# Optimization experiments

Measured on AMD Instinct MI355X. Metric: run time of the kernel, lower is better.

The kernel has to match this reference:

```python
import jax, jax.numpy as jnp
import numpy as np


def setup_inputs() -> dict:
    key = jax.random.key(0)
    ks = jax.random.split(key, 3)
    B, D, H, K = 16384, 256, 8192, 32
    x = jax.random.normal(ks[0], (B, D), dtype=jnp.float32)
    W_enc = jax.random.normal(ks[1], (H, D), dtype=jnp.float32) * (1.0 / np.sqrt(D))
    b_enc = jnp.zeros((H,), dtype=jnp.float32)
    # W_dec initialized as encoder weight clone, then row-normalized to unit norm
    W_dec = jax.random.normal(ks[2], (H, D), dtype=jnp.float32)
    W_dec = W_dec / (jnp.linalg.norm(W_dec, axis=1, keepdims=True) + jnp.finfo(jnp.float32).eps)
    b_dec = jnp.zeros((D,), dtype=jnp.float32)
    return {"x": x, "W_enc": W_enc, "b_enc": b_enc, "W_dec": W_dec, "b_dec": b_dec, "k": K}


def reference(x, W_enc, b_enc, W_dec, b_dec, k):
    B, D = x.shape
    H = W_enc.shape[0]
    # encoder: sae_in = x - b_dec; pre_acts = relu(Linear(sae_in))
    sae_in = x - b_dec
    pre_acts = jax.nn.relu(sae_in @ W_enc.T + b_enc)  # [B, H]
    # top-k activation over hidden dim
    topk_vals, topk_idx = jax.lax.top_k(pre_acts, k)  # [B, k]
    # per-latent activation counts (bincount over flattened indices)
    counts = jnp.zeros((H,), dtype=jnp.float32).at[topk_idx.reshape(-1)].add(1.0)
    # scatter top-k values into sparse latent tensor
    rows = jnp.arange(B)[:, None]
    z = jnp.zeros_like(pre_acts).at[rows, topk_idx].set(topk_vals)  # [B, H]
    # decode
    x_reconstructed = z @ W_dec + b_dec  # [B, D]
    # fvu stat
    e = x_reconstructed - x
    total_variance = jnp.sum((x - x.mean(0)) ** 2)
    fvu = jnp.sum(e ** 2) / total_variance
    return x_reconstructed, counts, fvu
```

## Files before the change

### kernel.cpp

```cpp
#include <hip/hip_runtime.h>

typedef unsigned short u16;
typedef unsigned int   u32;
typedef unsigned long long u64;

typedef __bf16 bf16x8 __attribute__((ext_vector_type(8)));
typedef float  f32x4  __attribute__((ext_vector_type(4)));

#define B_ROWS   16384
#define D_DIM    256
#define H_DIM    8192
#define THR_C    2.35f
#define QCAP     48

#define SAE_OFF    0u
#define WENCB_OFF  8388608u
#define WDECB_OFF  12582912u
#define TROW_OFF   16777216u
#define CAND_OFF   16842752u
#define CGQ_OFF    29425664u
#define COLSUM_OFF 29687808u
#define SUMSQ_OFF  29688832u
#define SSE_OFF    29688836u

__device__ __forceinline__ u16 f2bf(float f) {
  u32 u = __float_as_uint(f);
  u32 r = (u + 0x7fffu + ((u >> 16) & 1u)) >> 16;
  return (u16)r;
}
__device__ __forceinline__ float bf2f(u16 h) {
  return __uint_as_float(((u32)h) << 16);
}

__device__ __forceinline__ void async_copy16(const void* g, void* l) {
  __builtin_amdgcn_global_load_lds((const __attribute__((address_space(1))) u32*)g,
                                   (__attribute__((address_space(3))) u32*)l,
                                   16, 0, 0);
}

__global__ void k_zero(float* counts_out, float* accums) {
  int i = blockIdx.x * 256 + threadIdx.x;
  if (i < H_DIM + 1) counts_out[i] = 0.f;
  if (i < 258) accums[i] = 0.f;
}

__global__ __launch_bounds__(256) void k_prep_x(const float* __restrict__ x,
                                                const float* __restrict__ bdec,
                                                u16* __restrict__ sae,
                                                float* __restrict__ trow,
                                                float* __restrict__ colsum,
                                                float* __restrict__ sumsq) {
  __shared__ float cssh[256];
  __shared__ float sqsh[4];
  const int tid = threadIdx.x;
  const int l = tid & 63, w = tid >> 6;
  const float4 bd4 = *(const float4*)(bdec + l * 4);
  float4 cs4 = {0.f, 0.f, 0.f, 0.f};
  float sq = 0.f;
  for (int i = 0; i < 8; ++i) {
    const int row = blockIdx.x * 32 + w * 8 + i;
    const float4 x4 = *(const float4*)(x + (size_t)row * D_DIM + l * 4);
    float4 s4 = {x4.x - bd4.x, x4.y - bd4.y, x4.z - bd4.z, x4.w - bd4.w};
    ushort4 o;
    o.x = f2bf(s4.x); o.y = f2bf(s4.y); o.z = f2bf(s4.z); o.w = f2bf(s4.w);
    *(ushort4*)(sae + (size_t)row * D_DIM + l * 4) = o;
    cs4.x += x4.x; cs4.y += x4.y; cs4.z += x4.z; cs4.w += x4.w;
    sq += x4.x * x4.x + x4.y * x4.y + x4.z * x4.z + x4.w * x4.w;
    float ss = s4.x * s4.x + s4.y * s4.y + s4.z * s4.z + s4.w * s4.w;
#pragma unroll
    for (int off = 32; off > 0; off >>= 1) ss += __shfl_xor(ss, off);
    if (l == 0) trow[row] = THR_C * sqrtf(ss * (1.0f / 256.0f));
  }
  if (w == 0) { cssh[l * 4 + 0] = cs4.x; cssh[l * 4 + 1] = cs4.y; cssh[l * 4 + 2] = cs4.z; cssh[l * 4 + 3] = cs4.w; }
  __syncthreads();
#pragma unroll
  for (int ww = 1; ww < 4; ++ww) {
    if (w == ww) { cssh[l * 4 + 0] += cs4.x; cssh[l * 4 + 1] += cs4.y; cssh[l * 4 + 2] += cs4.z; cssh[l * 4 + 3] += cs4.w; }
    __syncthreads();
  }
#pragma unroll
  for (int off = 32; off > 0; off >>= 1) sq += __shfl_xor(sq, off);
  if (l == 0) sqsh[w] = sq;
  __syncthreads();
  atomicAdd(&colsum[tid], cssh[tid]);
  if (tid == 0) atomicAdd(sumsq, sqsh[0] + sqsh[1] + sqsh[2] + sqsh[3]);
}

__global__ __launch_bounds__(256) void k_prep_w(const float4* __restrict__ wenc,
                                                const float4* __restrict__ wdec,
                                                ushort4* __restrict__ wencb,
                                                ushort4* __restrict__ wdecb) {
  int i = blockIdx.x * 256 + threadIdx.x;
  const int half = H_DIM * D_DIM / 4;
  float4 v;
  if (i < half) v = wenc[i]; else v = wdec[i - half];
  ushort4 o;
  o.x = f2bf(v.x); o.y = f2bf(v.y); o.z = f2bf(v.z); o.w = f2bf(v.w);
  if (i < half) wencb[i] = o; else wdecb[i - half] = o;
}

__global__ __launch_bounds__(512, 4) void k_gemm(const u16* __restrict__ sae,
                                                 const u16* __restrict__ wenc,
                                                 const float* __restrict__ benc,
                                                 const float* __restrict__ trow,
                                                 u32* __restrict__ cand,
                                                 u32* __restrict__ cgq) {
  __shared__ __align__(16) u16 ldsw[2][8192];
  __shared__ u32 lcand[128 * QCAP];
  __shared__ u32 lcnt[128];
  const int tid = threadIdx.x;
  const int l   = tid & 63;
  const int w   = tid >> 6;
  const int bid = blockIdx.x;
  const int q   = bid & 3;
  const int m   = bid >> 2;
  const int wr  = w & 3;
  const int wc  = w >> 2;
  const int rbase = m * 128 + wr * 32;
  const int kc  = l >> 4;
  const int r16 = l & 15;

  if (tid < 128) lcnt[tid] = 0u;

  bf16x8 a[2][8];
#pragma unroll
  for (int fr = 0; fr < 2; ++fr) {
    const u16* ap = sae + (size_t)(rbase + fr * 16 + r16) * 256 + kc * 8;
#pragma unroll
    for (int ks = 0; ks < 8; ++ks)
      a[fr][ks] = *(const bf16x8*)(ap + ks * 32);
  }
  float trw[2][4];
#pragma unroll
  for (int fr = 0; fr < 2; ++fr)
#pragma unroll
    for (int rr = 0; rr < 4; ++rr)
      trw[fr][rr] = trow[rbase + fr * 16 + kc * 4 + rr];

  const char* wbytes = (const char*)wenc;
  auto stage = [&](int ci, int buf) {
    const int gcol0 = q * 2048 + ci * 32;
#pragma unroll
    for (int i = 0; i < 2; ++i) {
      int L    = i * 8192 + tid * 16;
      int col  = L >> 9;
      int pblk = (L >> 4) & 31;
      int cblk = pblk ^ (col & 15);
      const void* src = wbytes + (size_t)(gcol0 + col) * 512 + (size_t)cblk * 16;
      void* dst = (char*)(&ldsw[buf][0]) + i * 8192 + w * 1024;
      async_copy16(src, dst);
    }
  };

  stage(0, 0);
  __syncthreads();

  const f32x4 fzero = {0.f, 0.f, 0.f, 0.f};
  for (int ci = 0; ci < 64; ++ci) {
    const int cur = ci & 1;
    if (ci + 1 < 64) stage(ci + 1, cur ^ 1);
    const int gcol0 = q * 2048 + ci * 32;
    const char* bufc = (const char*)(&ldsw[cur][0]);

    const float be = benc[gcol0 + wc * 16 + r16];

    f32x4 acc[2];
    acc[0] = fzero; acc[1] = fzero;

#pragma unroll
    for (int ks = 0; ks < 8; ++ks) {
      const int colL = wc * 16 + r16;
      const int pb = (ks * 4 + kc) ^ r16;
      const bf16x8 bfrag = *(const bf16x8*)(bufc + (size_t)colL * 512 + (size_t)pb * 16);
#pragma unroll
      for (int fr = 0; fr < 2; ++fr)
        acc[fr] = __builtin_amdgcn_mfma_f32_16x16x32_bf16(a[fr][ks], bfrag, acc[fr], 0, 0, 0);
    }

#pragma unroll
    for (int fr = 0; fr < 2; ++fr) {
#pragma unroll
      for (int rr = 0; rr < 4; ++rr) {
        float v = acc[fr][rr] + be;
        if (v > trw[fr][rr]) {
          const int rowl = wr * 32 + fr * 16 + kc * 4 + rr;
          const int colg = gcol0 + wc * 16 + r16;
          u32 pos = atomicAdd(&lcnt[rowl], 1u);
          if (pos < (u32)QCAP)
            lcand[rowl * QCAP + pos] = ((u32)f2bf(v) << 16) | (u32)colg;
        }
      }
    }
    __syncthreads();
  }

  if (tid < 128) cgq[(size_t)(m * 128 + tid) * 4 + q] = lcnt[tid];
  const int rowl = tid >> 2;
  const u32 cnt = lcnt[rowl];
  const u32 lim = cnt < (u32)QCAP ? cnt : (u32)QCAP;
  u32* dst = cand + ((size_t)(m * 128 + rowl) * 4 + q) * QCAP;
#pragma unroll
  for (int j = 0; j < QCAP / 4; ++j) {
    const u32 s = (u32)(tid & 3) + 4u * j;
    if (s < lim) dst[s] = lcand[rowl * QCAP + s];
  }
}

__device__ __forceinline__ u64 sort64(u64 v, int l) {
#pragma unroll
  for (int k = 2; k <= 64; k <<= 1) {
#pragma unroll
    for (int j = k >> 1; j > 0; j >>= 1) {
      u64 o = __shfl_xor(v, j);
      const bool up    = ((l & k) == 0);
      const bool lower = ((l & j) == 0);
      u64 mn = v < o ? v : o;
      u64 mx = v < o ? o : v;
      v = (up == lower) ? mn : mx;
    }
  }
  return v;
}
__device__ __forceinline__ u32 sort64u(u32 v, int l) {
#pragma unroll
  for (int k = 2; k <= 64; k <<= 1) {
#pragma unroll
    for (int j = k >> 1; j > 0; j >>= 1) {
      u32 o = __shfl_xor(v, j);
      const bool up    = ((l & k) == 0);
      const bool lower = ((l & j) == 0);
      u32 mn = v < o ? v : o;
      u32 mx = v < o ? o : v;
      v = (up == lower) ? mn : mx;
    }
  }
  return v;
}

__global__ __launch_bounds__(256) void k_seldec(const u32* __restrict__ cand,
                                                const u32* __restrict__ cgq,
                                                const u16* __restrict__ sae,
                                                const u16* __restrict__ wenc,
                                                const float* __restrict__ benc,
                                                const float* __restrict__ wencf,
                                                const u16* __restrict__ wdecb,
                                                const float* __restrict__ bdec,
                                                const float* __restrict__ x,
                                                float* __restrict__ out,
                                                float* __restrict__ counts,
                                                float* __restrict__ sse) {
  __shared__ float sh_s[4][256];
  __shared__ float essh[4];
  const int l = threadIdx.x & 63;
  const int w = threadIdx.x >> 6;
  const int row = blockIdx.x * 4 + w;
  const float4 x4  = *(const float4*)(x + (size_t)row * D_DIM + l * 4);
  const float4 bd4 = *(const float4*)(bdec + l * 4);
  {
    float4 s4 = {x4.x - bd4.x, x4.y - bd4.y, x4.z - bd4.z, x4.w - bd4.w};
    *(float4*)(&sh_s[w][l * 4]) = s4;
  }

  const uint4 c4 = *(const uint4*)(cgq + (size_t)row * 4);
  const bool ovf = (c4.x > (u32)QCAP) | (c4.y > (u32)QCAP) | (c4.z > (u32)QCAP) | (c4.w > (u32)QCAP);
  const u32 cum0 = c4.x, cum1 = cum0 + c4.y, cum2 = cum1 + c4.z;
  const u32 T = cum2 + c4.w;
  u64 v;
  if (!ovf && T >= 32u) {
    const u32* cb = cand + (size_t)row * 4 * QCAP;
    auto fetch = [&](u32 p) -> u32 {
      u32 qi, off;
      if (p < cum0)      { qi = 0; off = p; }
      else if (p < cum1) { qi = 1; off = p - cum0; }
      else if (p < cum2) { qi = 2; off = p - cum1; }
      else               { qi = 3; off = p - cum2; }
      return cb[qi * QCAP + off];
    };
    u32 key = ((u32)l < T) ? fetch((u32)l) : 0u;
    key = sort64u(key, l);
    for (u32 p = 64; p < T; p += 64) {
      const u32 pp = p + (u32)l;
      u32 u = (pp < T) ? fetch(pp) : 0u;
      u = sort64u(u, l);
      u32 ur = __shfl(u, 63 - l);
      key = key > ur ? key : ur;
      key = sort64u(key, l);
    }
    v = key ? ((((u64)(key & 0xffff0000u)) << 32) | (u64)(key & 0x1fffu)) : 0ull;
    const int g  = l >> 4;
    const int gl = l & 15;
    const float* srow = &sh_s[w][gl * 16];
    const float4 sv0 = *(const float4*)(srow + 0);
    const float4 sv1 = *(const float4*)(srow + 4);
    const float4 sv2 = *(const float4*)(srow + 8);
    const float4 sv3 = *(const float4*)(srow + 12);
    auto cscore = [&](int j) -> float {
      const u32 kj = (u32)__shfl((int)key, 24 + g * 4 + j);
      const u32 ti = kj & 0x1fffu;
      const float* wrow = wencf + (size_t)ti * D_DIM + gl * 16;
      const float4 w0 = *(const float4*)(wrow + 0);
      const float4 w1 = *(const float4*)(wrow + 4);
      const float4 w2 = *(const float4*)(wrow + 8);
      const float4 w3 = *(const float4*)(wrow + 12);
      float p = sv0.x * w0.x + sv0.y * w0.y + sv0.z * w0.z + sv0.w * w0.w
              + sv1.x * w1.x + sv1.y * w1.y + sv1.z * w1.z + sv1.w * w1.w
              + sv2.x * w2.x + sv2.y * w2.y + sv2.z * w2.z + sv2.w * w2.w
              + sv3.x * w3.x + sv3.y * w3.y + sv3.z * w3.z + sv3.w * w3.w;
      p += __shfl_xor(p, 1);
      p += __shfl_xor(p, 2);
      p += __shfl_xor(p, 4);
      p += __shfl_xor(p, 8);
      return p;
    };
    const float r0 = cscore(0);
    const float r1 = cscore(1);
    const float r2 = cscore(2);
    const float r3 = cscore(3);
    {
      const int c  = (l - 24) & 63;
      const int sg = ((c >> 2) & 3) * 16;
      const float t0 = __shfl(r0, sg);
      const float t1 = __shfl(r1, sg);
      const float t2 = __shfl(r2, sg);
      const float t3 = __shfl(r3, sg);
      const int cm = c & 3;
      const float ps = cm == 0 ? t0 : (cm == 1 ? t1 : (cm == 2 ? t2 : t3));
      if (l >= 24 && l < 40 && key != 0u) {
        const u32 ti = key & 0x1fffu;
        const float ns = fmaxf(ps + benc[ti], 0.f);
        v = ((u64)__float_as_uint(ns) << 32) | ti;
      }
    }
    v = sort64(v, l);
  } else {
    v = 0ull;
    const u16* ap = sae + (size_t)row * 256;
    for (int c0 = 0; c0 < H_DIM; c0 += 64) {
      const int col = c0 + l;
      const u16* wp = wenc + (size_t)col * 256;
      float s = benc[col];
      for (int kk = 0; kk < 256; ++kk) s += bf2f(ap[kk]) * bf2f(wp[kk]);
      s = fmaxf(s, 0.f);
      u64 u = ((u64)__float_as_uint(s) << 32) | (u32)col;
      u = sort64(u, l);
      if (c0 == 0) {
        v = u;
      } else {
        u64 ur = __shfl(u, 63 - l);
        v = v > ur ? v : ur;
        v = sort64(v, l);
      }
    }
  }
  if (l >= 32) {
    const u32 idx = (u32)(v & 0xffffffffu);
    atomicAdd(&counts[idx], 1.0f);
  }
  float ax = 0.f, ay = 0.f, az = 0.f, aw2 = 0.f;
#pragma unroll 8
  for (int j = 0; j < 32; ++j) {
    const u64 t = __shfl(v, 32 + j);
    const float tv = __uint_as_float((u32)(t >> 32));
    const u32 ti = (u32)(t & 0x1fffu);
    const ushort4 wv = *(const ushort4*)(wdecb + (size_t)ti * 256 + l * 4);
    ax += tv * bf2f(wv.x); ay += tv * bf2f(wv.y);
    az += tv * bf2f(wv.z); aw2 += tv * bf2f(wv.w);
  }
  float4 xr;
  xr.x = ax + bd4.x; xr.y = ay + bd4.y; xr.z = az + bd4.z; xr.w = aw2 + bd4.w;
  *(float4*)(out + (size_t)row * 256 + l * 4) = xr;
  const float e0 = xr.x - x4.x, e1 = xr.y - x4.y, e2 = xr.z - x4.z, e3 = xr.w - x4.w;
  float es = e0 * e0 + e1 * e1 + e2 * e2 + e3 * e3;
#pragma unroll
  for (int off = 32; off > 0; off >>= 1) es += __shfl_xor(es, off);
  if (l == 0) essh[w] = es;
  __syncthreads();
  if (threadIdx.x == 0) atomicAdd(sse, essh[0] + essh[1] + essh[2] + essh[3]);
}

__global__ __launch_bounds__(256) void k_fvu(const float* __restrict__ colsum,
                                             const float* __restrict__ sumsq,
                                             const float* __restrict__ sse,
                                             float* __restrict__ out) {
  __shared__ float red[4];
  const int tid = threadIdx.x;
  const int l = tid & 63;
  const int w = tid >> 6;
  const float c = colsum[tid];
  float p = c * c;
#pragma unroll
  for (int off = 32; off > 0; off >>= 1) p += __shfl_xor(p, off);
  if (l == 0) red[w] = p;
  __syncthreads();
  if (tid == 0) {
    const float tv = sumsq[0] - (red[0] + red[1] + red[2] + red[3]) * (1.0f / 16384.0f);
    out[(size_t)B_ROWS * D_DIM + H_DIM] = sse[0] / tv;
  }
}

extern "C" void kernel_launch(void* const* d_in, const int* in_sizes, int n_in,
                              void* d_out, int out_size, void* d_ws, size_t ws_size,
                              hipStream_t stream) {
  (void)in_sizes; (void)n_in; (void)out_size; (void)ws_size;
  const float* x     = (const float*)d_in[0];
  const float* W_enc = (const float*)d_in[1];
  const float* b_enc = (const float*)d_in[2];
  const float* W_dec = (const float*)d_in[3];
  const float* b_dec = (const float*)d_in[4];
  float* out = (float*)d_out;
  char* ws = (char*)d_ws;

  u16*  sae    = (u16*)(ws + SAE_OFF);
  u16*  wencb  = (u16*)(ws + WENCB_OFF);
  u16*  wdecb  = (u16*)(ws + WDECB_OFF);
  float* trowp = (float*)(ws + TROW_OFF);
  u32*  candp  = (u32*)(ws + CAND_OFF);
  u32*  cgqp   = (u32*)(ws + CGQ_OFF);
  float* colsum = (float*)(ws + COLSUM_OFF);
  float* sumsq  = (float*)(ws + SUMSQ_OFF);
  float* ssep   = (float*)(ws + SSE_OFF);
  float* counts = out + (size_t)B_ROWS * D_DIM;

  hipLaunchKernelGGL(k_zero,   dim3(33),   dim3(256), 0, stream, counts, colsum);
  hipLaunchKernelGGL(k_prep_x, dim3(512),  dim3(256), 0, stream, x, b_dec, sae, trowp, colsum, sumsq);
  hipLaunchKernelGGL(k_prep_w, dim3(4096), dim3(256), 0, stream,
                     (const float4*)W_enc, (const float4*)W_dec, (ushort4*)wencb, (ushort4*)wdecb);
  hipLaunchKernelGGL(k_gemm,   dim3(512),  dim3(512), 0, stream, sae, wencb, b_enc, trowp, candp, cgqp);
  hipLaunchKernelGGL(k_seldec, dim3(4096), dim3(256), 0, stream, candp, cgqp, sae, wencb, b_enc, W_enc, wdecb, b_dec, x, out, counts, ssep);
  hipLaunchKernelGGL(k_fvu,    dim3(1),    dim3(256), 0, stream, colsum, sumsq, ssep, out);
}
```

Baseline: 217.0 us.

## Switch encoder GEMM to 32x32x16 MFMA with 256-row tiles per block

The encoder GEMM now uses 32x32x16 bf16 MFMA instructions, with two independent accumulators that are summed in the epilogue. The block row tile grows from 128 to 256 rows: each wave owns 32 rows across all 32 columns of a chunk, and the grid is halved. Each staged W_enc tile is reused across twice as many rows, cutting LDS and global weight traffic per output, and the larger MFMA shape gives better throughput per instruction. In exchange it holds more registers (16 A fragments and two 16-wide accumulators), uses more LDS for the candidate lists, and lowers the occupancy hint to 2, with only 256 blocks to fill the GPU.

```diff
diff --git a/kernel.cpp b/kernel.cpp
--- a/kernel.cpp
+++ b/kernel.cpp
@@ -6,6 +6,7 @@
 
 typedef __bf16 bf16x8 __attribute__((ext_vector_type(8)));
 typedef float  f32x4  __attribute__((ext_vector_type(4)));
+typedef float  f32x16 __attribute__((ext_vector_type(16)));
 
 #define B_ROWS   16384
 #define D_DIM    256
@@ -99,43 +100,37 @@
   if (i < half) wencb[i] = o; else wdecb[i - half] = o;
 }
 
-__global__ __launch_bounds__(512, 4) void k_gemm(const u16* __restrict__ sae,
+__global__ __launch_bounds__(512, 2) void k_gemm(const u16* __restrict__ sae,
                                                  const u16* __restrict__ wenc,
                                                  const float* __restrict__ benc,
                                                  const float* __restrict__ trow,
                                                  u32* __restrict__ cand,
                                                  u32* __restrict__ cgq) {
   __shared__ __align__(16) u16 ldsw[2][8192];
-  __shared__ u32 lcand[128 * QCAP];
-  __shared__ u32 lcnt[128];
+  __shared__ u32 lcand[256 * QCAP];
+  __shared__ u32 lcnt[256];
   const int tid = threadIdx.x;
   const int l   = tid & 63;
   const int w   = tid >> 6;
-  const int bid = blockIdx.x;
-  const int q   = bid & 3;
-  const int m   = bid >> 2;
-  const int wr  = w & 3;
-  const int wc  = w >> 2;
-  const int rbase = m * 128 + wr * 32;
-  const int kc  = l >> 4;
-  const int r16 = l & 15;
-
-  if (tid < 128) lcnt[tid] = 0u;
-
-  bf16x8 a[2][8];
-#pragma unroll
-  for (int fr = 0; fr < 2; ++fr) {
-    const u16* ap = sae + (size_t)(rbase + fr * 16 + r16) * 256 + kc * 8;
-#pragma unroll
-    for (int ks = 0; ks < 8; ++ks)
-      a[fr][ks] = *(const bf16x8*)(ap + ks * 32);
-  }
-  float trw[2][4];
-#pragma unroll
-  for (int fr = 0; fr < 2; ++fr)
-#pragma unroll
-    for (int rr = 0; rr < 4; ++rr)
-      trw[fr][rr] = trow[rbase + fr * 16 + kc * 4 + rr];
+  const int q   = blockIdx.x & 3;
+  const int m   = blockIdx.x >> 2;
+  const int rbase = m * 256 + w * 32;
+  const int r32 = l & 31;
+  const int h   = l >> 5;
+
+  if (tid < 256) lcnt[tid] = 0u;
+
+  bf16x8 a[16];
+  {
+    const u16* ap = sae + (size_t)(rbase + r32) * 256 + h * 8;
+#pragma unroll
+    for (int ks = 0; ks < 16; ++ks)
+      a[ks] = *(const bf16x8*)(ap + ks * 16);
+  }
+  float trw[16];
+#pragma unroll
+  for (int r = 0; r < 16; ++r)
+    trw[r] = trow[rbase + (r & 3) + 8 * (r >> 2) + 4 * h];
 
   const char* wbytes = (const char*)wenc;
   auto stage = [&](int ci, int buf) {
@@ -155,53 +150,47 @@
   stage(0, 0);
   __syncthreads();
 
-  const f32x4 fzero = {0.f, 0.f, 0.f, 0.f};
   for (int ci = 0; ci < 64; ++ci) {
     const int cur = ci & 1;
     if (ci + 1 < 64) stage(ci + 1, cur ^ 1);
     const int gcol0 = q * 2048 + ci * 32;
     const char* bufc = (const char*)(&ldsw[cur][0]);
 
-    const float be = benc[gcol0 + wc * 16 + r16];
-
-    f32x4 acc[2];
-    acc[0] = fzero; acc[1] = fzero;
-
-#pragma unroll
-    for (int ks = 0; ks < 8; ++ks) {
-      const int colL = wc * 16 + r16;
-      const int pb = (ks * 4 + kc) ^ r16;
-      const bf16x8 bfrag = *(const bf16x8*)(bufc + (size_t)colL * 512 + (size_t)pb * 16);
-#pragma unroll
-      for (int fr = 0; fr < 2; ++fr)
-        acc[fr] = __builtin_amdgcn_mfma_f32_16x16x32_bf16(a[fr][ks], bfrag, acc[fr], 0, 0, 0);
-    }
-
-#pragma unroll
-    for (int fr = 0; fr < 2; ++fr) {
-#pragma unroll
-      for (int rr = 0; rr < 4; ++rr) {
-        float v = acc[fr][rr] + be;
-        if (v > trw[fr][rr]) {
-          const int rowl = wr * 32 + fr * 16 + kc * 4 + rr;
-          const int colg = gcol0 + wc * 16 + r16;
-          u32 pos = atomicAdd(&lcnt[rowl], 1u);
-          if (pos < (u32)QCAP)
-            lcand[rowl * QCAP + pos] = ((u32)f2bf(v) << 16) | (u32)colg;
-        }
+    const float be = benc[gcol0 + r32];
+
+    f32x16 acc0 = {0.f}, acc1 = {0.f};
+#pragma unroll
+    for (int ks = 0; ks < 16; ks += 2) {
+      const int pb0 = ((ks + 0) * 2 + h) ^ (l & 15);
+      const int pb1 = ((ks + 1) * 2 + h) ^ (l & 15);
+      const bf16x8 b0 = *(const bf16x8*)(bufc + (size_t)r32 * 512 + (size_t)pb0 * 16);
+      const bf16x8 b1 = *(const bf16x8*)(bufc + (size_t)r32 * 512 + (size_t)pb1 * 16);
+      acc0 = __builtin_amdgcn_mfma_f32_32x32x16_bf16(a[ks + 0], b0, acc0, 0, 0, 0);
+      acc1 = __builtin_amdgcn_mfma_f32_32x32x16_bf16(a[ks + 1], b1, acc1, 0, 0, 0);
+    }
+
+#pragma unroll
+    for (int r = 0; r < 16; ++r) {
+      const float v = acc0[r] + acc1[r] + be;
+      if (v > trw[r]) {
+        const int rowl = w * 32 + (r & 3) + 8 * (r >> 2) + 4 * h;
+        const int colg = gcol0 + r32;
+        u32 pos = atomicAdd(&lcnt[rowl], 1u);
+        if (pos < (u32)QCAP)
+          lcand[rowl * QCAP + pos] = ((u32)f2bf(v) << 16) | (u32)colg;
       }
     }
     __syncthreads();
   }
 
-  if (tid < 128) cgq[(size_t)(m * 128 + tid) * 4 + q] = lcnt[tid];
-  const int rowl = tid >> 2;
+  if (tid < 256) cgq[(size_t)(m * 256 + tid) * 4 + q] = lcnt[tid];
+  const int rowl = tid >> 1;
   const u32 cnt = lcnt[rowl];
   const u32 lim = cnt < (u32)QCAP ? cnt : (u32)QCAP;
-  u32* dst = cand + ((size_t)(m * 128 + rowl) * 4 + q) * QCAP;
-#pragma unroll
-  for (int j = 0; j < QCAP / 4; ++j) {
-    const u32 s = (u32)(tid & 3) + 4u * j;
+  u32* dst = cand + ((size_t)(m * 256 + rowl) * 4 + q) * QCAP;
+#pragma unroll
+  for (int j = 0; j < QCAP / 2; ++j) {
+    const u32 s = (u32)(tid & 1) + 2u * j;
     if (s < lim) dst[s] = lcand[rowl * QCAP + s];
   }
 }
@@ -425,7 +414,7 @@
   hipLaunchKernelGGL(k_prep_x, dim3(512),  dim3(256), 0, stream, x, b_dec, sae, trowp, colsum, sumsq);
   hipLaunchKernelGGL(k_prep_w, dim3(4096), dim3(256), 0, stream,
                      (const float4*)W_enc, (const float4*)W_dec, (ushort4*)wencb, (ushort4*)wdecb);
-  hipLaunchKernelGGL(k_gemm,   dim3(512),  dim3(512), 0, stream, sae, wencb, b_enc, trowp, candp, cgqp);
+  hipLaunchKernelGGL(k_gemm,   dim3(256),  dim3(512), 0, stream, sae, wencb, b_enc, trowp, candp, cgqp);
   hipLaunchKernelGGL(k_seldec, dim3(4096), dim3(256), 0, stream, candp, cgqp, sae, wencb, b_enc, W_enc, wdecb, b_dec, x, out, counts, ssep);
   hipLaunchKernelGGL(k_fvu,    dim3(1),    dim3(256), 0, stream, colsum, sumsq, ssep, out);
 }
```

Result: slower. 249.3 us (+14.9%).

## Retile encoder GEMM to 256-row blocks over 8 column splits

Applied to the files above, without the earlier changes.

The encoder GEMM now gives each block 256 rows and one eighth of the hidden columns, using 4 waves of 64 rows each instead of 8 waves of 32 rows. Each block stages 16 weight columns per step, so every B fragment loaded from LDS feeds four MFMAs instead of two, and the LDS staging buffers shrink. The candidate buffer is split into 8 per-row segments with a smaller per-segment cap, and the select kernel is updated to read the 8 counts and index across the 8 segments. The smaller cap makes per-segment overflow more likely, which sends those rows to the slow exact fallback path. The higher register use of the larger A tile may also reduce occupancy.

```diff
diff --git a/kernel.cpp b/kernel.cpp
--- a/kernel.cpp
+++ b/kernel.cpp
@@ -11,17 +11,17 @@
 #define D_DIM    256
 #define H_DIM    8192
 #define THR_C    2.35f
-#define QCAP     48
+#define QCAP     28
 
 #define SAE_OFF    0u
 #define WENCB_OFF  8388608u
 #define WDECB_OFF  12582912u
 #define TROW_OFF   16777216u
 #define CAND_OFF   16842752u
-#define CGQ_OFF    29425664u
-#define COLSUM_OFF 29687808u
-#define SUMSQ_OFF  29688832u
-#define SSE_OFF    29688836u
+#define CGQ_OFF    31522816u
+#define COLSUM_OFF 32047104u
+#define SUMSQ_OFF  32048128u
+#define SSE_OFF    32048132u
 
 __device__ __forceinline__ u16 f2bf(float f) {
   u32 u = __float_as_uint(f);
@@ -99,55 +99,52 @@
   if (i < half) wencb[i] = o; else wdecb[i - half] = o;
 }
 
-__global__ __launch_bounds__(512, 4) void k_gemm(const u16* __restrict__ sae,
+__global__ __launch_bounds__(256, 2) void k_gemm(const u16* __restrict__ sae,
                                                  const u16* __restrict__ wenc,
                                                  const float* __restrict__ benc,
                                                  const float* __restrict__ trow,
                                                  u32* __restrict__ cand,
                                                  u32* __restrict__ cgq) {
-  __shared__ __align__(16) u16 ldsw[2][8192];
-  __shared__ u32 lcand[128 * QCAP];
-  __shared__ u32 lcnt[128];
+  __shared__ __align__(16) u16 ldsw[2][4096];
+  __shared__ u32 lcand[256 * QCAP];
+  __shared__ u32 lcnt[256];
   const int tid = threadIdx.x;
   const int l   = tid & 63;
   const int w   = tid >> 6;
-  const int bid = blockIdx.x;
-  const int q   = bid & 3;
-  const int m   = bid >> 2;
-  const int wr  = w & 3;
-  const int wc  = w >> 2;
-  const int rbase = m * 128 + wr * 32;
+  const int q   = blockIdx.x & 7;
+  const int m   = blockIdx.x >> 3;
+  const int rbase = m * 256 + w * 64;
   const int kc  = l >> 4;
   const int r16 = l & 15;
 
-  if (tid < 128) lcnt[tid] = 0u;
-
-  bf16x8 a[2][8];
-#pragma unroll
-  for (int fr = 0; fr < 2; ++fr) {
+  lcnt[tid] = 0u;
+
+  bf16x8 a[4][8];
+#pragma unroll
+  for (int fr = 0; fr < 4; ++fr) {
     const u16* ap = sae + (size_t)(rbase + fr * 16 + r16) * 256 + kc * 8;
 #pragma unroll
     for (int ks = 0; ks < 8; ++ks)
       a[fr][ks] = *(const bf16x8*)(ap + ks * 32);
   }
-  float trw[2][4];
-#pragma unroll
-  for (int fr = 0; fr < 2; ++fr)
+  float trw[4][4];
+#pragma unroll
+  for (int fr = 0; fr < 4; ++fr)
 #pragma unroll
     for (int rr = 0; rr < 4; ++rr)
       trw[fr][rr] = trow[rbase + fr * 16 + kc * 4 + rr];
 
   const char* wbytes = (const char*)wenc;
   auto stage = [&](int ci, int buf) {
-    const int gcol0 = q * 2048 + ci * 32;
+    const int gcol0 = q * 1024 + ci * 16;
 #pragma unroll
     for (int i = 0; i < 2; ++i) {
-      int L    = i * 8192 + tid * 16;
+      int L    = i * 4096 + tid * 16;
       int col  = L >> 9;
       int pblk = (L >> 4) & 31;
-      int cblk = pblk ^ (col & 15);
+      int cblk = pblk ^ col;
       const void* src = wbytes + (size_t)(gcol0 + col) * 512 + (size_t)cblk * 16;
-      void* dst = (char*)(&ldsw[buf][0]) + i * 8192 + w * 1024;
+      void* dst = (char*)(&ldsw[buf][0]) + i * 4096 + w * 1024;
       async_copy16(src, dst);
     }
   };
@@ -159,32 +156,32 @@
   for (int ci = 0; ci < 64; ++ci) {
     const int cur = ci & 1;
     if (ci + 1 < 64) stage(ci + 1, cur ^ 1);
-    const int gcol0 = q * 2048 + ci * 32;
+    const int gcol0 = q * 1024 + ci * 16;
     const char* bufc = (const char*)(&ldsw[cur][0]);
 
-    const float be = benc[gcol0 + wc * 16 + r16];
-
-    f32x4 acc[2];
-    acc[0] = fzero; acc[1] = fzero;
+    const float be = benc[gcol0 + r16];
+
+    f32x4 acc[4];
+#pragma unroll
+    for (int fr = 0; fr < 4; ++fr) acc[fr] = fzero;
 
 #pragma unroll
     for (int ks = 0; ks < 8; ++ks) {
-      const int colL = wc * 16 + r16;
       const int pb = (ks * 4 + kc) ^ r16;
-      const bf16x8 bfrag = *(const bf16x8*)(bufc + (size_t)colL * 512 + (size_t)pb * 16);
-#pragma unroll
-      for (int fr = 0; fr < 2; ++fr)
+      const bf16x8 bfrag = *(const bf16x8*)(bufc + (size_t)r16 * 512 + (size_t)pb * 16);
+#pragma unroll
+      for (int fr = 0; fr < 4; ++fr)
         acc[fr] = __builtin_amdgcn_mfma_f32_16x16x32_bf16(a[fr][ks], bfrag, acc[fr], 0, 0, 0);
     }
 
 #pragma unroll
-    for (int fr = 0; fr < 2; ++fr) {
+    for (int fr = 0; fr < 4; ++fr) {
 #pragma unroll
       for (int rr = 0; rr < 4; ++rr) {
         float v = acc[fr][rr] + be;
         if (v > trw[fr][rr]) {
-          const int rowl = wr * 32 + fr * 16 + kc * 4 + rr;
-          const int colg = gcol0 + wc * 16 + r16;
+          const int rowl = w * 64 + fr * 16 + kc * 4 + rr;
+          const int colg = gcol0 + r16;
           u32 pos = atomicAdd(&lcnt[rowl], 1u);
           if (pos < (u32)QCAP)
             lcand[rowl * QCAP + pos] = ((u32)f2bf(v) << 16) | (u32)colg;
@@ -194,16 +191,11 @@
     __syncthreads();
   }
 
-  if (tid < 128) cgq[(size_t)(m * 128 + tid) * 4 + q] = lcnt[tid];
-  const int rowl = tid >> 2;
-  const u32 cnt = lcnt[rowl];
+  cgq[(size_t)(m * 256 + tid) * 8 + q] = lcnt[tid];
+  const u32 cnt = lcnt[tid];
   const u32 lim = cnt < (u32)QCAP ? cnt : (u32)QCAP;
-  u32* dst = cand + ((size_t)(m * 128 + rowl) * 4 + q) * QCAP;
-#pragma unroll
-  for (int j = 0; j < QCAP / 4; ++j) {
-    const u32 s = (u32)(tid & 3) + 4u * j;
-    if (s < lim) dst[s] = lcand[rowl * QCAP + s];
-  }
+  u32* dst = cand + ((size_t)(m * 256 + tid) * 8 + q) * QCAP;
+  for (u32 s = 0; s < lim; ++s) dst[s] = lcand[tid * QCAP + s];
 }
 
 __device__ __forceinline__ u64 sort64(u64 v, int l) {
@@ -261,19 +253,25 @@
     *(float4*)(&sh_s[w][l * 4]) = s4;
   }
 
-  const uint4 c4 = *(const uint4*)(cgq + (size_t)row * 4);
-  const bool ovf = (c4.x > (u32)QCAP) | (c4.y > (u32)QCAP) | (c4.z > (u32)QCAP) | (c4.w > (u32)QCAP);
-  const u32 cum0 = c4.x, cum1 = cum0 + c4.y, cum2 = cum1 + c4.z;
-  const u32 T = cum2 + c4.w;
+  const uint4 ca = *(const uint4*)(cgq + (size_t)row * 8);
+  const uint4 cz = *(const uint4*)(cgq + (size_t)row * 8 + 4);
+  const bool ovf = (ca.x > (u32)QCAP) | (ca.y > (u32)QCAP) | (ca.z > (u32)QCAP) | (ca.w > (u32)QCAP)
+                 | (cz.x > (u32)QCAP) | (cz.y > (u32)QCAP) | (cz.z > (u32)QCAP) | (cz.w > (u32)QCAP);
+  const u32 c0 = ca.x,      c1 = c0 + ca.y, c2 = c1 + ca.z, c3 = c2 + ca.w;
+  const u32 c4s = c3 + cz.x, c5 = c4s + cz.y, c6 = c5 + cz.z;
+  const u32 T  = c6 + cz.w;
   u64 v;
   if (!ovf && T >= 32u) {
-    const u32* cb = cand + (size_t)row * 4 * QCAP;
+    const u32* cb = cand + (size_t)row * 8 * QCAP;
     auto fetch = [&](u32 p) -> u32 {
       u32 qi, off;
-      if (p < cum0)      { qi = 0; off = p; }
-      else if (p < cum1) { qi = 1; off = p - cum0; }
-      else if (p < cum2) { qi = 2; off = p - cum1; }
-      else               { qi = 3; off = p - cum2; }
+      if (p < c3) {
+        if (p < c1) { if (p < c0) { qi = 0; off = p; } else { qi = 1; off = p - c0; } }
+        else        { if (p < c2) { qi = 2; off = p - c1; } else { qi = 3; off = p - c2; } }
+      } else {
+        if (p < c5) { if (p < c4s) { qi = 4; off = p - c3; } else { qi = 5; off = p - c4s; } }
+        else        { if (p < c6)  { qi = 6; off = p - c5; } else { qi = 7; off = p - c6; } }
+      }
       return cb[qi * QCAP + off];
     };
     u32 key = ((u32)l < T) ? fetch((u32)l) : 0u;
@@ -335,15 +333,15 @@
   } else {
     v = 0ull;
     const u16* ap = sae + (size_t)row * 256;
-    for (int c0 = 0; c0 < H_DIM; c0 += 64) {
-      const int col = c0 + l;
+    for (int cc0 = 0; cc0 < H_DIM; cc0 += 64) {
+      const int col = cc0 + l;
       const u16* wp = wenc + (size_t)col * 256;
       float s = benc[col];
       for (int kk = 0; kk < 256; ++kk) s += bf2f(ap[kk]) * bf2f(wp[kk]);
       s = fmaxf(s, 0.f);
       u64 u = ((u64)__float_as_uint(s) << 32) | (u32)col;
       u = sort64(u, l);
-      if (c0 == 0) {
+      if (cc0 == 0) {
         v = u;
       } else {
         u64 ur = __shfl(u, 63 - l);
@@ -425,7 +423,7 @@
   hipLaunchKernelGGL(k_prep_x, dim3(512),  dim3(256), 0, stream, x, b_dec, sae, trowp, colsum, sumsq);
   hipLaunchKernelGGL(k_prep_w, dim3(4096), dim3(256), 0, stream,
                      (const float4*)W_enc, (const float4*)W_dec, (ushort4*)wencb, (ushort4*)wdecb);
-  hipLaunchKernelGGL(k_gemm,   dim3(512),  dim3(512), 0, stream, sae, wencb, b_enc, trowp, candp, cgqp);
+  hipLaunchKernelGGL(k_gemm,   dim3(512),  dim3(256), 0, stream, sae, wencb, b_enc, trowp, candp, cgqp);
   hipLaunchKernelGGL(k_seldec, dim3(4096), dim3(256), 0, stream, candp, cgqp, sae, wencb, b_enc, W_enc, wdecb, b_dec, x, out, counts, ssep);
   hipLaunchKernelGGL(k_fvu,    dim3(1),    dim3(256), 0, stream, colsum, sumsq, ssep, out);
 }
```

After: 238.4 us. 9.8% more time.
